# Kernel tuning notes

Measured on AMD Instinct MI355X. Metric: run time of the kernel, lower is better.

The kernel has to match this reference:

```python
import jax, jax.numpy as jnp
import numpy as np

B, N, D = 2, 128, 128          # batch, nodes, dim
DE = 64                        # dim_edge_refinement
H, DH = 8, 32                  # heads, per-head dim
DI = H * DH                    # dim_inner = dim * dim_head = 256
DMI = 2 * DI                   # mlp_expansion_factor * dim_inner = 512
MD = 2                         # max_degree
S = 1 + 2 * MD                 # value/edge channel groups = 5
FFD = 512                      # int(2.0 * dim * 2) for EquivariantFeedForward


def _ln(x, g, eps=1e-5):
    mu = x.mean(-1, keepdims=True)
    var = ((x - mu) ** 2).mean(-1, keepdims=True)
    return (x - mu) / jnp.sqrt(var + eps) * g


def setup_inputs() -> dict:
    key = jax.random.key(0)
    ks = iter(jax.random.split(key, 64))
    def rn(shape, scale=1.0):
        return jax.random.normal(next(ks), shape, dtype=jnp.float32) * scale
    w = 0.05
    return dict(
        h=rn((B, N, D)), x1=rn((B, N, D, 3)), x2=rn((B, N, D, 5)),
        t_ij=rn((B, N, N, D)), r1=rn((B, N, N, 3)), r2=rn((B, N, N, 5)),
        g_i=jnp.ones((D,), jnp.float32), g_j=jnp.ones((D,), jnp.float32),
        Wq=rn((D, DI), w), Wk=rn((D, DI), w),
        Wv1=rn((D, DMI), w), bv1=jnp.zeros((DMI,), jnp.float32),
        Wv2=rn((DMI, S * DI), w), bv2=jnp.zeros((S * DI,), jnp.float32),
        Wp1=rn((D, DMI), w), bp1=jnp.zeros((DMI,), jnp.float32),
        Wp2=rn((DMI, S * DI), w), bp2=jnp.zeros((S * DI,), jnp.float32),
        Wek=rn((D, S * DI), w), Wev=rn((D, S * DI), w),
        Wcomb=rn((DI, D), w),
        Wqh=rn((D, DE), w), Wk1h=rn((D, DE), w), Wk2h=rn((D, DE), w),
        Wep=rn((2 * DE, D), w), Wres=rn((D, D), w),
        P1=rn((D, D), w), P2=rn((D, D), w),
        Wf1a=rn((2 * D, FFD), w), bf1a=jnp.zeros((FFD,), jnp.float32),
        Wf2a=rn((FFD, 2 * D), w), bf2a=jnp.zeros((2 * D,), jnp.float32),
        Wf1b=rn((2 * D, FFD), w), bf1b=jnp.zeros((FFD,), jnp.float32),
        Wf2b=rn((FFD, 2 * D), w), bf2b=jnp.zeros((2 * D,), jnp.float32),
    )


def reference(h, x1, x2, t_ij, r1, r2, g_i, g_j, Wq, Wk, Wv1, bv1, Wv2, bv2,
              Wp1, bp1, Wp2, bp2, Wek, Wev, Wcomb, Wqh, Wk1h, Wk2h, Wep, Wres,
              P1, P2, Wf1a, bf1a, Wf2a, bf2a, Wf1b, bf1b, Wf2b, bf2b):
    # ---- HierarchicalTensorRefinement: per-degree inner products -> edge refresh
    q1 = jnp.einsum('bndm,de->bnem', x1, Wqh)
    q2 = jnp.einsum('bndm,de->bnem', x2, Wqh)
    k1 = jnp.einsum('bndm,de->bnem', x1, Wk1h)
    k2 = jnp.einsum('bndm,de->bnem', x2, Wk2h)
    w_ij = jnp.concatenate([
        jnp.einsum('biem,bjem->bije', q1, k1),
        jnp.einsum('biem,bjem->bije', q2, k2)], axis=-1)       # [b,n,n,2*DE]
    t = w_ij @ Wep + t_ij @ Wres                                # [b,n,n,D]
    # ---- GeometryAwareTensorAttention
    hi = _ln(h, g_i)
    hj = _ln(h, g_j)
    q = (hi @ Wq).reshape(B, N, H, DH).transpose(0, 2, 1, 3)    # bhnd
    k = (hj @ Wk).reshape(B, N, H, DH).transpose(0, 2, 1, 3)
    v = (jax.nn.silu(hj @ Wv1 + bv1) @ Wv2 + bv2).reshape(B, N, S, H, DH).transpose(0, 3, 1, 2, 4)   # bhnsd
    pv = (jax.nn.silu(hj @ Wp1 + bp1) @ Wp2 + bp2).reshape(B, N, S, H, DH).transpose(0, 3, 1, 2, 4)
    ek = jax.nn.silu(t @ Wek).reshape(B, N, N, S, H, DH).transpose(0, 4, 1, 2, 3, 5)                  # bhijsd
    ev = (t @ Wev).reshape(B, N, N, S, H, DH).transpose(0, 4, 1, 2, 3, 5)
    sim_num = jnp.einsum('bhid,bhjd->bhij', q, k)
    sim_den = jnp.einsum('bhid,bhijsd->bhis', q, ek)            # edge-keyed denominator
    attn = sim_num[..., None] / sim_den[:, :, :, None, :]       # bhijs
    sea = attn[..., None] * v[:, :, None] + ev * pv[:, :, None]  # bhijsd
    out = sea.transpose(0, 2, 3, 4, 1, 5).reshape(B, N, N, S, H * DH) @ Wcomb  # [b,i,j,S,D]
    h_sc = out[..., 0, :]              # [b,i,j,D]
    r_sc = out[..., 1:1 + MD, :]       # [b,i,j,MD,D]
    x_sc = out[..., 1 + MD:, :]        # [b,i,j,MD,D]
    h2 = h + h_sc.sum(axis=2)
    x1a = jnp.einsum('bjdm,bijd->bidm', x1, x_sc[..., 0, :]) + jnp.einsum('bijm,bijd->bidm', r1, r_sc[..., 0, :])
    x2a = jnp.einsum('bjdm,bijd->bidm', x2, x_sc[..., 1, :]) + jnp.einsum('bijm,bijd->bidm', r2, r_sc[..., 1, :])
    # ---- EquivariantFeedForward (eq 13)
    def ff_branch(xl, P, W1, b1, W2, b2):
        proj = jnp.einsum('bndm,de->bnem', xl, P)
        inv = jnp.sqrt((proj ** 2).sum(-1) + 1e-12)             # invariant norm over m
        mo = jax.nn.silu(jnp.concatenate([h2, inv], -1) @ W1 + b1) @ W2 + b2
        m1, m2 = jnp.split(mo, 2, axis=-1)
        return m1, proj * m2[..., None]
    m1a, xr1 = ff_branch(x1a, P1, Wf1a, bf1a, Wf2a, bf2a)
    m1b, xr2 = ff_branch(x2a, P2, Wf1b, bf1b, Wf2b, bf2b)
    h3 = h2 + m1a + m1b
    x1f = x1a + xr1
    x2f = x2a + xr2
    # pack outputs: h [b,n,d,1] | x1 [b,n,d,3] | x2 [b,n,d,5] -> [b,n,d,9]
    return jnp.concatenate([h3[..., None], x1f, x2f], axis=-1)
```

## Files before the change

kernel.cpp:

```cpp
#include <hip/hip_runtime.h>
#include <math.h>

#define OFF_Q    0
#define OFF_K    65536
#define OFF_A1V  131072
#define OFF_A1P  262144
#define OFF_V    393216
#define OFF_PV   720896
#define OFF_VW   1048576
#define OFF_QK   2359296
#define OFF_T    2621440
#define OFF_DEN  6815744
#define OFF_ACC  6825984
#define OFF_WEVT 7940096
#define OFF_WCT  8022016
#define OFF_HI   8038400
#define OFF_HJ   8071168

typedef __bf16 bf16x8 __attribute__((ext_vector_type(8)));
typedef float  f32x4  __attribute__((ext_vector_type(4)));

__device__ __forceinline__ float silu_f(float x){
  return x / (1.0f + __expf(-x));
}
__device__ __forceinline__ unsigned short f2bf(float x){
  union{float f; unsigned u;} c; c.f = x;
  unsigned r = c.u + 0x7FFFu + ((c.u >> 16) & 1u);
  return (unsigned short)(r >> 16);
}
__device__ __forceinline__ unsigned packbf(float a, float b){
  return (unsigned)f2bf(a) | ((unsigned)f2bf(b) << 16);
}

__global__ __launch_bounds__(128) void k0a_ln(
    const float* __restrict__ h, const float* __restrict__ g_i, const float* __restrict__ g_j,
    float* __restrict__ ws)
{
  __shared__ float red[2];
  const int r = blockIdx.x, tid = threadIdx.x;
  const int w = tid >> 6, l = tid & 63;
  const float hv = h[r*128 + tid];
  float s = hv;
  #pragma unroll
  for (int o = 1; o < 64; o <<= 1) s += __shfl_xor(s, o);
  if (l == 0) red[w] = s;
  __syncthreads();
  const float mu = (red[0] + red[1]) * (1.f/128.f);
  const float dv = hv - mu;
  float s2 = dv*dv;
  #pragma unroll
  for (int o = 1; o < 64; o <<= 1) s2 += __shfl_xor(s2, o);
  __syncthreads();
  if (l == 0) red[w] = s2;
  __syncthreads();
  const float rstd = 1.0f / sqrtf((red[0] + red[1])*(1.f/128.f) + 1e-5f);
  ws[OFF_HI + r*128 + tid] = dv * rstd * g_i[tid];
  ws[OFF_HJ + r*128 + tid] = dv * rstd * g_j[tid];
  if (tid < 40) ws[OFF_DEN + r*40 + tid] = 0.f;
}

__global__ __launch_bounds__(256) void k0b_qkv(
    const float* __restrict__ Wq, const float* __restrict__ Wk,
    const float* __restrict__ Wv1, const float* __restrict__ bv1,
    const float* __restrict__ Wp1, const float* __restrict__ bp1,
    float* __restrict__ ws)
{
  __shared__ float hrow[128];
  const int bid = blockIdx.x;
  const int row = bid / 6, ch = bid - 6*(bid/6);
  const int tid = threadIdx.x;
  if (tid < 128) hrow[tid] = ws[((ch == 0) ? OFF_HI : OFF_HJ) + row*128 + tid];
  __syncthreads();
  const float* W; int c; float bias = 0.f; bool act = false; float* dst; int wstride;
  switch(ch){
    case 0: W = Wq;  c = tid;      wstride = 256; dst = ws + OFF_Q   + row*256 + c; break;
    case 1: W = Wk;  c = tid;      wstride = 256; dst = ws + OFF_K   + row*256 + c; break;
    case 2: W = Wv1; c = tid;      wstride = 512; bias = bv1[c]; act = true; dst = ws + OFF_A1V + row*512 + c; break;
    case 3: W = Wv1; c = 256+tid;  wstride = 512; bias = bv1[c]; act = true; dst = ws + OFF_A1V + row*512 + c; break;
    case 4: W = Wp1; c = tid;      wstride = 512; bias = bp1[c]; act = true; dst = ws + OFF_A1P + row*512 + c; break;
    default:W = Wp1; c = 256+tid;  wstride = 512; bias = bp1[c]; act = true; dst = ws + OFF_A1P + row*512 + c; break;
  }
  float acc = bias;
  #pragma unroll 8
  for (int d = 0; d < 128; ++d) acc += hrow[d] * W[d*wstride + c];
  *dst = act ? silu_f(acc) : acc;
}

__global__ __launch_bounds__(256) void k0c_qk12(
    const float* __restrict__ x1, const float* __restrict__ x2,
    const float* __restrict__ Wqh, const float* __restrict__ Wk1h, const float* __restrict__ Wk2h,
    float* __restrict__ ws)
{
  __shared__ float x1r[384], x2r[640];
  const int row = blockIdx.x, tid = threadIdx.x;
  for (int idx = tid; idx < 384; idx += 256) x1r[idx] = x1[row*384 + idx];
  for (int idx = tid; idx < 640; idx += 256) x2r[idx] = x2[row*640 + idx];
  __syncthreads();
  for (int idx = tid; idx < 512; idx += 256){
    if (idx < 192){
      const int e = idx/3, m = idx - e*3;
      float qa = 0.f, ka = 0.f;
      #pragma unroll 8
      for (int d = 0; d < 128; ++d){
        const float xv = x1r[d*3 + m];
        qa += xv*Wqh[d*64 + e];
        ka += xv*Wk1h[d*64 + e];
      }
      ws[OFF_QK + row*1024 + idx] = qa;
      ws[OFF_QK + row*1024 + 512 + idx] = ka;
    } else {
      const int i2 = idx - 192;
      const int e = i2/5, m = i2 - e*5;
      float qa = 0.f, ka = 0.f;
      #pragma unroll 8
      for (int d = 0; d < 128; ++d){
        const float xv = x2r[d*5 + m];
        qa += xv*Wqh[d*64 + e];
        ka += xv*Wk2h[d*64 + e];
      }
      ws[OFF_QK + row*1024 + 192 + i2] = qa;
      ws[OFF_QK + row*1024 + 704 + i2] = ka;
    }
  }
}

__global__ __launch_bounds__(256) void k1_vp(
    const float* __restrict__ Wv2, const float* __restrict__ bv2,
    const float* __restrict__ Wp2, const float* __restrict__ bp2,
    float* __restrict__ ws)
{
  __shared__ float A[512][16];
  __shared__ float Bc[64][128];
  const int tid = threadIdx.x;
  const int rt = blockIdx.x & 31;
  const int ct = blockIdx.x >> 5;
  const int r0 = rt*16;
  const bool isP = (r0 >= 256);
  const int rbase = isP ? (r0 - 256) : r0;
  const float* __restrict__ src  = ws + (isP ? OFF_A1P : OFF_A1V);
  const float* __restrict__ W    = isP ? Wp2 : Wv2;
  const float* __restrict__ bias = isP ? bp2 : bv2;
  const int c0 = ct*128;
  for (int idx = tid; idx < 2048; idx += 256){
    const int rl = idx & 15;
    const int c4 = (idx >> 4) * 4;
    const float4 v = *(const float4*)&src[(rbase+rl)*512 + c4];
    A[c4+0][rl] = v.x; A[c4+1][rl] = v.y; A[c4+2][rl] = v.z; A[c4+3][rl] = v.w;
  }
  float acc[4][2] = {{0.f}};
  const int rg = tid & 3;
  const int cg = tid >> 2;
  for (int kc = 0; kc < 8; ++kc){
    __syncthreads();
    for (int idx = tid; idx < 2048; idx += 256){
      const int kl = idx >> 5;
      const int c4 = (idx & 31)*4;
      *(float4*)&Bc[kl][c4] = *(const float4*)&W[(kc*64+kl)*1280 + c0 + c4];
    }
    __syncthreads();
    #pragma unroll 8
    for (int k = 0; k < 64; ++k){
      const float4 a = *(const float4*)&A[kc*64+k][rg*4];
      const float b0 = Bc[k][cg*2], b1 = Bc[k][cg*2+1];
      acc[0][0] += a.x*b0; acc[0][1] += a.x*b1;
      acc[1][0] += a.y*b0; acc[1][1] += a.y*b1;
      acc[2][0] += a.z*b0; acc[2][1] += a.z*b1;
      acc[3][0] += a.w*b0; acc[3][1] += a.w*b1;
    }
  }
  float* __restrict__ dst = ws + (isP ? OFF_PV : OFF_V);
  for (int rr = 0; rr < 4; ++rr)
    for (int cc = 0; cc < 2; ++cc){
      const int c = c0 + cg*2 + cc;
      dst[(rbase + rg*4 + rr)*1280 + c] = acc[rr][cc] + bias[c];
    }
}

__global__ __launch_bounds__(256) void k2_vw(const float* __restrict__ Wcomb, float* __restrict__ ws)
{
  __shared__ float vr[1280];
  const int j = blockIdx.x, tid = threadIdx.x;
  for (int idx = tid; idx < 320; idx += 256)
    *(float4*)&vr[idx*4] = *(const float4*)&ws[OFF_V + j*1280 + idx*4];
  __syncthreads();
  const int d = tid & 127;
  for (int sh = tid >> 7; sh < 40; sh += 2){
    const int s = sh >> 3, hh = sh & 7;
    float a = 0.f;
    #pragma unroll 8
    for (int dh = 0; dh < 32; ++dh)
      a += vr[s*256 + hh*32 + dh] * Wcomb[(hh*32+dh)*128 + d];
    ws[OFF_VW + j*5120 + sh*128 + d] = a;
  }
}

__global__ __launch_bounds__(256) void k_cvt(
    const float* __restrict__ Wev, const float* __restrict__ Wcomb, float* __restrict__ ws)
{
  __shared__ float ld[16][256];
  const int tid = threadIdx.x;
  if (blockIdx.x < 80){
    const int c0 = blockIdx.x*16;
    for (int p = 0; p < 8; ++p){
      const int idx = tid + p*256;
      const int k = idx >> 4, cl = idx & 15;
      ld[cl][k] = Wev[k*1280 + c0 + cl];
    }
    __syncthreads();
    const int cl = tid >> 4, k8 = tid & 15;
    uint4 u;
    u.x = packbf(ld[cl][k8*8+0], ld[cl][k8*8+1]);
    u.y = packbf(ld[cl][k8*8+2], ld[cl][k8*8+3]);
    u.z = packbf(ld[cl][k8*8+4], ld[cl][k8*8+5]);
    u.w = packbf(ld[cl][k8*8+6], ld[cl][k8*8+7]);
    ((uint4*)(ws + OFF_WEVT))[(c0+cl)*16 + k8] = u;
  } else {
    const int c0 = (blockIdx.x - 80)*16;
    for (int p = 0; p < 16; ++p){
      const int idx = tid + p*256;
      const int k = idx >> 4, cl = idx & 15;
      ld[cl][k] = Wcomb[k*128 + c0 + cl];
    }
    __syncthreads();
    const int cl = tid >> 4, k8i = tid & 15;
    for (int pass = 0; pass < 2; ++pass){
      const int k8 = k8i + pass*16;
      uint4 u;
      u.x = packbf(ld[cl][k8*8+0], ld[cl][k8*8+1]);
      u.y = packbf(ld[cl][k8*8+2], ld[cl][k8*8+3]);
      u.z = packbf(ld[cl][k8*8+4], ld[cl][k8*8+5]);
      u.w = packbf(ld[cl][k8*8+6], ld[cl][k8*8+7]);
      ((uint4*)(ws + OFF_WCT))[(c0+cl)*32 + k8] = u;
    }
  }
}

__global__ __launch_bounds__(512) void k3_t(
    const float* __restrict__ t_ij, const float* __restrict__ Wep, const float* __restrict__ Wres,
    float* __restrict__ ws)
{
  __shared__ float A[256][64];
  __shared__ float bufB[8192];
  __shared__ float qrow[512];
  const int tid = threadIdx.x;
  const int bi = blockIdx.x >> 1;
  const int jt = blockIdx.x & 1;
  const int j0 = jt*64;
  const int b  = bi >> 7;
  if (tid < 128) *(float4*)&qrow[tid*4] = *(const float4*)&ws[OFF_QK + bi*1024 + tid*4];
  for (int idx = tid; idx < 2048; idx += 512){
    const int jl = idx >> 5;
    const int d4 = (idx & 31)*4;
    const float4 v = *(const float4*)&t_ij[(bi*128 + j0 + jl)*128 + d4];
    A[128+d4+0][jl] = v.x; A[128+d4+1][jl] = v.y; A[128+d4+2][jl] = v.z; A[128+d4+3][jl] = v.w;
  }
  float* kst = bufB;
  for (int jq = 0; jq < 4; ++jq){
    __syncthreads();
    for (int idx = tid; idx < 2048; idx += 512){
      const int jl = idx & 15;
      const int c4 = (idx >> 4)*4;
      const float4 v = *(const float4*)&ws[OFF_QK + (b*128 + j0 + jq*16 + jl)*1024 + 512 + c4];
      kst[(c4+0)*16 + jl] = v.x; kst[(c4+1)*16 + jl] = v.y;
      kst[(c4+2)*16 + jl] = v.z; kst[(c4+3)*16 + jl] = v.w;
    }
    __syncthreads();
    for (int idx = tid; idx < 2048; idx += 512){
      const int jl = idx & 15;
      const int e  = idx >> 4;
      float acc = 0.f;
      if (e < 64){
        #pragma unroll
        for (int m = 0; m < 3; ++m) acc += qrow[e*3+m] * kst[(e*3+m)*16 + jl];
      } else {
        const int e2 = e - 64;
        #pragma unroll
        for (int m = 0; m < 5; ++m) acc += qrow[192 + e2*5+m] * kst[(192 + e2*5+m)*16 + jl];
      }
      A[e][jq*16 + jl] = acc;
    }
  }
  float acc[4][4] = {{0.f}};
  const int jg = tid & 15;
  const int cg = tid >> 4;
  float* Bc = bufB;
  for (int kc = 0; kc < 4; ++kc){
    __syncthreads();
    for (int idx = tid; idx < 2048; idx += 512){
      const int kl = idx >> 5;
      const int c4 = (idx & 31)*4;
      const int k = kc*64 + kl;
      const float* srcw = (k < 128) ? &Wep[k*128 + c4] : &Wres[(k-128)*128 + c4];
      *(float4*)&Bc[kl*128 + c4] = *(const float4*)srcw;
    }
    __syncthreads();
    #pragma unroll 2
    for (int kl = 0; kl < 64; ++kl){
      const float4 a = *(const float4*)&A[kc*64+kl][jg*4];
      const float2 bA = *(const float2*)&Bc[kl*128 + cg*2];
      const float2 bB = *(const float2*)&Bc[kl*128 + 64 + cg*2];
      const float av[4] = {a.x,a.y,a.z,a.w};
      #pragma unroll
      for (int r = 0; r < 4; ++r){
        acc[r][0] += av[r]*bA.x; acc[r][1] += av[r]*bA.y;
        acc[r][2] += av[r]*bB.x; acc[r][3] += av[r]*bB.y;
      }
    }
  }
  __syncthreads();
  for (int jj = 0; jj < 4; ++jj){
    bufB[(jg*4+jj)*128 + cg*2+0]    = acc[jj][0];
    bufB[(jg*4+jj)*128 + cg*2+1]    = acc[jj][1];
    bufB[(jg*4+jj)*128 + 64+cg*2+0] = acc[jj][2];
    bufB[(jg*4+jj)*128 + 64+cg*2+1] = acc[jj][3];
  }
  __syncthreads();
  for (int idx = tid; idx < 2048; idx += 512){
    const int jl = idx >> 5;
    const int c4 = (idx & 31)*4;
    *(float4*)&ws[OFF_T + (bi*128 + j0 + jl)*128 + c4] = *(const float4*)&bufB[jl*128 + c4];
  }
}

__global__ __launch_bounds__(256) void k4_den(
    const float* __restrict__ Wek, float* __restrict__ ws)
{
  __shared__ float tl[128][64];
  __shared__ float wl[128][64];
  __shared__ float den[40];
  __shared__ float ql[256];
  const int tid = threadIdx.x;
  const int bi = blockIdx.x >> 1;
  const int jh = blockIdx.x & 1;
  const int j0 = jh*64;
  for (int idx = tid; idx < 2048; idx += 256){
    const int jl = idx >> 5;
    const int c4 = (idx & 31)*4;
    const float4 v = *(const float4*)&ws[OFF_T + (bi*128 + j0 + jl)*128 + c4];
    tl[c4+0][jl] = v.x; tl[c4+1][jl] = v.y; tl[c4+2][jl] = v.z; tl[c4+3][jl] = v.w;
  }
  if (tid < 40) den[tid] = 0.f;
  ql[tid] = ws[OFF_Q + bi*256 + tid];
  const int jg = tid & 15;
  const int cg = tid >> 4;
  for (int ch = 0; ch < 20; ++ch){
    __syncthreads();
    for (int idx = tid; idx < 2048; idx += 256){
      const int kl = idx >> 4;
      const int c4 = (idx & 15)*4;
      *(float4*)&wl[kl][c4] = *(const float4*)&Wek[kl*1280 + ch*64 + c4];
    }
    __syncthreads();
    float acc[4][4] = {{0.f}};
    #pragma unroll 2
    for (int k = 0; k < 128; ++k){
      const float4 a = *(const float4*)&tl[k][jg*4];
      const float4 w = *(const float4*)&wl[k][cg*4];
      const float av[4] = {a.x,a.y,a.z,a.w};
      #pragma unroll
      for (int r = 0; r < 4; ++r){
        acc[r][0] += av[r]*w.x; acc[r][1] += av[r]*w.y;
        acc[r][2] += av[r]*w.z; acc[r][3] += av[r]*w.w;
      }
    }
    #pragma unroll
    for (int cc = 0; cc < 4; ++cc){
      const int col = ch*64 + cg*4 + cc;
      float cs = silu_f(acc[0][cc]) + silu_f(acc[1][cc]) + silu_f(acc[2][cc]) + silu_f(acc[3][cc]);
      cs += __shfl_xor(cs, 1, 16);
      cs += __shfl_xor(cs, 2, 16);
      cs += __shfl_xor(cs, 4, 16);
      cs += __shfl_xor(cs, 8, 16);
      if (jg == 0){
        const int s  = col >> 8;
        const int hd = col & 255;
        atomicAdd(&den[(hd>>5)*5 + s], ql[hd]*cs);
      }
    }
  }
  __syncthreads();
  if (tid < 40) atomicAdd(&ws[OFF_DEN + bi*40 + tid], den[tid]);
}

__global__ __launch_bounds__(512, 4) void k5_pass2(
    const float* __restrict__ x1, const float* __restrict__ x2,
    const float* __restrict__ r1, const float* __restrict__ r2,
    float* __restrict__ ws)
{
  __shared__ unsigned short tA[8192];
  __shared__ unsigned short wevB[8192];
  __shared__ unsigned short wcombB[8192];
  __shared__ unsigned short epB[4096];
  __shared__ float num[8][64];
  __shared__ float acc17[17*128];
  __shared__ float ql[256];
  __shared__ float rdenl[40];

  const int tid  = threadIdx.x;
  const int lane = tid & 63;
  const int w    = tid >> 6;
  const int wm   = w & 3;
  const int wn   = w >> 2;
  const int l15  = lane & 15;
  const int kq   = lane >> 4;

  const int bi = blockIdx.x >> 1;
  const int jh = blockIdx.x & 1;
  const int j0 = jh*64;
  const int b  = bi >> 7;

  #pragma unroll
  for (int p = 0; p < 4; ++p){
    const int idx = tid + p*512;
    const int j = idx >> 5;
    const int d4 = (idx & 31)*4;
    const float4 v = *(const float4*)&ws[OFF_T + (bi*128 + j0 + j)*128 + d4];
    uint2 u;
    u.x = packbf(v.x, v.y);
    u.y = packbf(v.z, v.w);
    *(uint2*)((char*)tA + j*256 + ((d4*2) ^ ((j&7)<<4))) = u;
  }
  if (tid < 64) *(float4*)&ql[tid*4] = *(const float4*)&ws[OFF_Q + bi*256 + tid*4];
  if (tid < 40) rdenl[tid] = 1.0f / ws[OFF_DEN + bi*40 + tid];
  for (int idx = tid; idx < 17*128; idx += 512) acc17[idx] = 0.f;
  __syncthreads();

  {
    const int hh = tid >> 6, jl = tid & 63;
    const float* krow = &ws[OFF_K + (b*128 + j0 + jl)*256 + hh*32];
    float a = 0.f;
    #pragma unroll
    for (int dh = 0; dh < 32; ++dh) a += ql[hh*32+dh]*krow[dh];
    num[hh][jl] = a;
  }

  const int jA = wm*16 + l15;
  bf16x8 af[4];
  #pragma unroll
  for (int ks = 0; ks < 4; ++ks)
    af[ks] = *(const bf16x8*)((const char*)tA + jA*256 + ((ks*64 + kq*16) ^ ((jA&7)<<4)));

  const uint4* wevt = (const uint4*)(ws + OFF_WEVT);
  const uint4* wct  = (const uint4*)(ws + OFF_WCT);

  for (int s = 0; s < 5; ++s){
    f32x4 o0 = {0,0,0,0}, o1 = {0,0,0,0}, o2 = {0,0,0,0}, o3 = {0,0,0,0};
    for (int ch4 = 0; ch4 < 4; ++ch4){
      __syncthreads();
      #pragma unroll
      for (int p = 0; p < 2; ++p){
        const int idx = tid + p*512;
        const int cl = idx & 63, kg = idx >> 6;
        const uint4 v = wevt[(s*256 + ch4*64 + cl)*16 + kg];
        *(uint4*)((char*)wevB + cl*256 + ((kg*16) ^ ((cl&7)<<4))) = v;
      }
      #pragma unroll
      for (int p = 0; p < 2; ++p){
        const int idx = tid + p*512;
        const int hg = idx & 7, d = idx >> 3;
        const uint4 v = wct[d*32 + ch4*8 + hg];
        *(uint4*)((char*)wcombB + d*128 + ((hg*16) ^ ((d&7)<<4))) = v;
      }
      __syncthreads();
      f32x4 ev0 = {0,0,0,0}, ev1 = {0,0,0,0};
      {
        const int c0l = wn*32 + l15;
        const int c1l = c0l + 16;
        #pragma unroll
        for (int ks = 0; ks < 4; ++ks){
          const bf16x8 b0 = *(const bf16x8*)((const char*)wevB + c0l*256 + ((ks*64 + kq*16) ^ ((c0l&7)<<4)));
          const bf16x8 b1 = *(const bf16x8*)((const char*)wevB + c1l*256 + ((ks*64 + kq*16) ^ ((c1l&7)<<4)));
          ev0 = __builtin_amdgcn_mfma_f32_16x16x32_bf16(af[ks], b0, ev0, 0, 0, 0);
          ev1 = __builtin_amdgcn_mfma_f32_16x16x32_bf16(af[ks], b1, ev1, 0, 0, 0);
        }
      }
      #pragma unroll
      for (int nt = 0; nt < 2; ++nt){
        const int cl = wn*32 + nt*16 + l15;
        const int cglob = s*256 + ch4*64 + cl;
        #pragma unroll
        for (int r = 0; r < 4; ++r){
          const int jl = wm*16 + kq*4 + r;
          const float pvv = ws[OFF_PV + (b*128 + j0 + jl)*1280 + cglob];
          const float evv = (nt == 0) ? ev0[r] : ev1[r];
          *(unsigned short*)((char*)epB + jl*128 + ((cl*2) ^ ((jl&7)<<4))) = f2bf(evv * pvv);
        }
      }
      __syncthreads();
      #pragma unroll
      for (int ks = 0; ks < 2; ++ks){
        const bf16x8 a = *(const bf16x8*)((const char*)epB + jA*128 + ((ks*64 + kq*16) ^ ((jA&7)<<4)));
        #pragma unroll
        for (int nt = 0; nt < 4; ++nt){
          const int dl = wn*64 + nt*16 + l15;
          const bf16x8 bb = *(const bf16x8*)((const char*)wcombB + dl*128 + ((ks*64 + kq*16) ^ ((dl&7)<<4)));
          if      (nt == 0) o0 = __builtin_amdgcn_mfma_f32_16x16x32_bf16(a, bb, o0, 0, 0, 0);
          else if (nt == 1) o1 = __builtin_amdgcn_mfma_f32_16x16x32_bf16(a, bb, o1, 0, 0, 0);
          else if (nt == 2) o2 = __builtin_amdgcn_mfma_f32_16x16x32_bf16(a, bb, o2, 0, 0, 0);
          else              o3 = __builtin_amdgcn_mfma_f32_16x16x32_bf16(a, bb, o3, 0, 0, 0);
        }
      }
    }
    #pragma unroll
    for (int r = 0; r < 4; ++r){
      const int jl = wm*16 + kq*4 + r;
      const float* vwbase = ws + OFF_VW + (b*128 + j0 + jl)*5120 + s*1024 + wn*64 + l15;
      #pragma unroll
      for (int hh = 0; hh < 8; ++hh){
        const float at = num[hh][jl] * rdenl[hh*5 + s];
        const float* vp = vwbase + hh*128;
        o0[r] += at * vp[0];
        o1[r] += at * vp[16];
        o2[r] += at * vp[32];
        o3[r] += at * vp[48];
      }
    }
    if (s == 0){
      #pragma unroll
      for (int nt = 0; nt < 4; ++nt){
        const f32x4 oo = (nt==0)?o0:(nt==1)?o1:(nt==2)?o2:o3;
        float p = oo[0] + oo[1] + oo[2] + oo[3];
        p += __shfl_xor(p, 16);
        p += __shfl_xor(p, 32);
        if (lane < 16) atomicAdd(&acc17[wn*64 + nt*16 + lane], p);
      }
    } else if (s <= 2){
      const int M = (s == 1) ? 3 : 5;
      const int slot0 = (s == 1) ? 1 : 4;
      const float* rw = (s == 1) ? r1 : r2;
      for (int m = 0; m < M; ++m){
        float wj[4];
        #pragma unroll
        for (int r = 0; r < 4; ++r)
          wj[r] = rw[(bi*128 + j0 + wm*16 + kq*4 + r)*M + m];
        #pragma unroll
        for (int nt = 0; nt < 4; ++nt){
          const f32x4 oo = (nt==0)?o0:(nt==1)?o1:(nt==2)?o2:o3;
          float p = wj[0]*oo[0] + wj[1]*oo[1] + wj[2]*oo[2] + wj[3]*oo[3];
          p += __shfl_xor(p, 16);
          p += __shfl_xor(p, 32);
          if (lane < 16) atomicAdd(&acc17[(slot0+m)*128 + wn*64 + nt*16 + lane], p);
        }
      }
    } else {
      const int M = (s == 3) ? 3 : 5;
      const int slot0 = (s == 3) ? 9 : 12;
      const float* xw = (s == 3) ? x1 : x2;
      for (int m = 0; m < M; ++m){
        #pragma unroll
        for (int nt = 0; nt < 4; ++nt){
          const int d = wn*64 + nt*16 + l15;
          const f32x4 oo = (nt==0)?o0:(nt==1)?o1:(nt==2)?o2:o3;
          float p = 0.f;
          #pragma unroll
          for (int r = 0; r < 4; ++r)
            p += xw[((b*128 + j0 + wm*16 + kq*4 + r)*128 + d)*M + m] * oo[r];
          p += __shfl_xor(p, 16);
          p += __shfl_xor(p, 32);
          if (lane < 16) atomicAdd(&acc17[(slot0+m)*128 + d], p);
        }
      }
    }
  }
  __syncthreads();
  for (int idx = tid; idx < 2176; idx += 512)
    ws[OFF_ACC + (bi*2 + jh)*2176 + idx] = acc17[idx];
}

__global__ __launch_bounds__(256) void k6_tail(
    const float* __restrict__ h,
    const float* __restrict__ P1, const float* __restrict__ P2,
    const float* __restrict__ Wf1a, const float* __restrict__ bf1a,
    const float* __restrict__ Wf2a, const float* __restrict__ bf2a,
    const float* __restrict__ Wf1b, const float* __restrict__ bf1b,
    const float* __restrict__ Wf2b, const float* __restrict__ bf2b,
    const float* __restrict__ ws, float* __restrict__ out)
{
  __shared__ float a17[2176];
  __shared__ float h2s[128];
  __shared__ float x1a[384], x2a[640];
  __shared__ float pj1[384], pj2[640];
  __shared__ float inv1[128], inv2[128];
  __shared__ float za[512], zb[512];
  __shared__ float m1a[128], m2a[128], m1b[128], m2b[128];
  const int tid = threadIdx.x;
  const int row = blockIdx.x;
  for (int idx = tid; idx < 2176; idx += 256)
    a17[idx] = ws[OFF_ACC + (row*2)*2176 + idx] + ws[OFF_ACC + (row*2+1)*2176 + idx];
  __syncthreads();
  if (tid < 128) h2s[tid] = h[row*128 + tid] + a17[tid];
  for (int idx = tid; idx < 384; idx += 256){
    const int d = idx/3, m = idx - d*3;
    x1a[idx] = a17[(1+m)*128 + d] + a17[(9+m)*128 + d];
  }
  for (int idx = tid; idx < 640; idx += 256){
    const int d = idx/5, m = idx - d*5;
    x2a[idx] = a17[(4+m)*128 + d] + a17[(12+m)*128 + d];
  }
  __syncthreads();
  if (tid < 128){
    const int e = tid;
    float pa[3] = {0.f,0.f,0.f};
    for (int d = 0; d < 128; ++d){
      const float p = P1[d*128 + e];
      pa[0] += x1a[d*3+0]*p;
      pa[1] += x1a[d*3+1]*p;
      pa[2] += x1a[d*3+2]*p;
    }
    pj1[e*3+0] = pa[0]; pj1[e*3+1] = pa[1]; pj1[e*3+2] = pa[2];
    inv1[e] = sqrtf(pa[0]*pa[0] + pa[1]*pa[1] + pa[2]*pa[2] + 1e-12f);
  } else {
    const int e = tid - 128;
    float pa[5] = {0.f,0.f,0.f,0.f,0.f};
    for (int d = 0; d < 128; ++d){
      const float p = P2[d*128 + e];
      pa[0] += x2a[d*5+0]*p;
      pa[1] += x2a[d*5+1]*p;
      pa[2] += x2a[d*5+2]*p;
      pa[3] += x2a[d*5+3]*p;
      pa[4] += x2a[d*5+4]*p;
    }
    #pragma unroll
    for (int m = 0; m < 5; ++m) pj2[e*5+m] = pa[m];
    inv2[e] = sqrtf(pa[0]*pa[0]+pa[1]*pa[1]+pa[2]*pa[2]+pa[3]*pa[3]+pa[4]*pa[4] + 1e-12f);
  }
  __syncthreads();
  for (int it = 0; it < 2; ++it){
    const int f = tid + it*256;
    float av = bf1a[f], bv_ = bf1b[f];
    #pragma unroll 4
    for (int k = 0; k < 128; ++k){
      av  += h2s[k]*Wf1a[k*512 + f];
      bv_ += h2s[k]*Wf1b[k*512 + f];
    }
    #pragma unroll 4
    for (int k = 0; k < 128; ++k){
      av  += inv1[k]*Wf1a[(128+k)*512 + f];
      bv_ += inv2[k]*Wf1b[(128+k)*512 + f];
    }
    za[f] = silu_f(av); zb[f] = silu_f(bv_);
  }
  __syncthreads();
  {
    const int g = tid;
    float am = bf2a[g], bm = bf2b[g];
    #pragma unroll 4
    for (int f = 0; f < 512; ++f){
      am += za[f]*Wf2a[f*256 + g];
      bm += zb[f]*Wf2b[f*256 + g];
    }
    if (g < 128){ m1a[g] = am; m1b[g] = bm; }
    else        { m2a[g-128] = am; m2b[g-128] = bm; }
  }
  __syncthreads();
  if (tid < 128){
    const int d = tid;
    const int ob = (row*128 + d)*9;
    out[ob+0] = h2s[d] + m1a[d] + m1b[d];
    #pragma unroll
    for (int m = 0; m < 3; ++m)
      out[ob+1+m] = x1a[d*3+m] + pj1[d*3+m]*m2a[d];
    #pragma unroll
    for (int m = 0; m < 5; ++m)
      out[ob+4+m] = x2a[d*5+m] + pj2[d*5+m]*m2b[d];
  }
}

extern "C" void kernel_launch(void* const* d_in, const int* in_sizes, int n_in,
                              void* d_out, int out_size, void* d_ws, size_t ws_size,
                              hipStream_t stream)
{
  (void)in_sizes; (void)n_in; (void)out_size; (void)ws_size;
  const float* h    = (const float*)d_in[0];
  const float* x1   = (const float*)d_in[1];
  const float* x2   = (const float*)d_in[2];
  const float* t_ij = (const float*)d_in[3];
  const float* r1   = (const float*)d_in[4];
  const float* r2   = (const float*)d_in[5];
  const float* g_i  = (const float*)d_in[6];
  const float* g_j  = (const float*)d_in[7];
  const float* Wq   = (const float*)d_in[8];
  const float* Wk   = (const float*)d_in[9];
  const float* Wv1  = (const float*)d_in[10];
  const float* bv1  = (const float*)d_in[11];
  const float* Wv2  = (const float*)d_in[12];
  const float* bv2  = (const float*)d_in[13];
  const float* Wp1  = (const float*)d_in[14];
  const float* bp1  = (const float*)d_in[15];
  const float* Wp2  = (const float*)d_in[16];
  const float* bp2  = (const float*)d_in[17];
  const float* Wek  = (const float*)d_in[18];
  const float* Wev  = (const float*)d_in[19];
  const float* Wcomb= (const float*)d_in[20];
  const float* Wqh  = (const float*)d_in[21];
  const float* Wk1h = (const float*)d_in[22];
  const float* Wk2h = (const float*)d_in[23];
  const float* Wep  = (const float*)d_in[24];
  const float* Wres = (const float*)d_in[25];
  const float* P1   = (const float*)d_in[26];
  const float* P2   = (const float*)d_in[27];
  const float* Wf1a = (const float*)d_in[28];
  const float* bf1a = (const float*)d_in[29];
  const float* Wf2a = (const float*)d_in[30];
  const float* bf2a = (const float*)d_in[31];
  const float* Wf1b = (const float*)d_in[32];
  const float* bf1b = (const float*)d_in[33];
  const float* Wf2b = (const float*)d_in[34];
  const float* bf2b = (const float*)d_in[35];
  float* ws  = (float*)d_ws;
  float* out = (float*)d_out;

  k0a_ln <<<dim3(256),  dim3(128), 0, stream>>>(h, g_i, g_j, ws);
  k0b_qkv<<<dim3(1536), dim3(256), 0, stream>>>(Wq, Wk, Wv1, bv1, Wp1, bp1, ws);
  k0c_qk12<<<dim3(256), dim3(256), 0, stream>>>(x1, x2, Wqh, Wk1h, Wk2h, ws);
  k1_vp  <<<dim3(320),  dim3(256), 0, stream>>>(Wv2, bv2, Wp2, bp2, ws);
  k2_vw  <<<dim3(256),  dim3(256), 0, stream>>>(Wcomb, ws);
  k_cvt  <<<dim3(88),   dim3(256), 0, stream>>>(Wev, Wcomb, ws);
  k3_t   <<<dim3(512),  dim3(512), 0, stream>>>(t_ij, Wep, Wres, ws);
  k4_den <<<dim3(512),  dim3(256), 0, stream>>>(Wek, ws);
  k5_pass2<<<dim3(512), dim3(512), 0, stream>>>(x1, x2, r1, r2, ws);
  k6_tail<<<dim3(256),  dim3(256), 0, stream>>>(h, P1, P2, Wf1a, bf1a, Wf2a, bf2a, Wf1b, bf1b, Wf2b, bf2b, ws, out);
}
```

Before: 746.9 us.

## Restructure edge GEMMs with swizzled LDS and register-streamed weights, split den over columns

k3_t and k4_den now keep only the activation tile in shared memory, using an XOR-swizzled layout to avoid bank conflicts. Weights are read straight from global memory with one-step register prefetch instead of being staged through LDS. k4_den is split across five 256-column groups, giving a 2560-block grid with 64 accumulators per thread, and the per-head reductions are done in shared memory before the global atomics. The aim is to cut LDS traffic and barriers and raise parallelism, at the cost of more register pressure and repeated global weight reads per block.

```diff
diff --git a/kernel.cpp b/kernel.cpp
--- a/kernel.cpp
+++ b/kernel.cpp
@@ -30,6 +30,12 @@
 }
 __device__ __forceinline__ unsigned packbf(float a, float b){
   return (unsigned)f2bf(a) | ((unsigned)f2bf(b) << 16);
+}
+__device__ __forceinline__ void swz_store(float* Abase, int k, int j, float v){
+  *(float*)((char*)Abase + k*256 + ((((j>>2) ^ ((k>>2)&15))) << 4) + ((j&3)<<2)) = v;
+}
+__device__ __forceinline__ f32x4 swz_load4(const float* Abase, int k, int chunk){
+  return *(const f32x4*)((const char*)Abase + k*256 + ((chunk ^ ((k>>2)&15)) << 4));
 }
 
 __global__ __launch_bounds__(128) void k0a_ln(
@@ -235,26 +241,19 @@
   }
 }
 
-__global__ __launch_bounds__(512) void k3_t(
+__global__ __launch_bounds__(512, 2) void k3_t(
     const float* __restrict__ t_ij, const float* __restrict__ Wep, const float* __restrict__ Wres,
     float* __restrict__ ws)
 {
-  __shared__ float A[256][64];
-  __shared__ float bufB[8192];
+  __shared__ float A[16384];
   __shared__ float qrow[512];
+  float* kst = A + 8192;
   const int tid = threadIdx.x;
   const int bi = blockIdx.x >> 1;
   const int jt = blockIdx.x & 1;
   const int j0 = jt*64;
   const int b  = bi >> 7;
   if (tid < 128) *(float4*)&qrow[tid*4] = *(const float4*)&ws[OFF_QK + bi*1024 + tid*4];
-  for (int idx = tid; idx < 2048; idx += 512){
-    const int jl = idx >> 5;
-    const int d4 = (idx & 31)*4;
-    const float4 v = *(const float4*)&t_ij[(bi*128 + j0 + jl)*128 + d4];
-    A[128+d4+0][jl] = v.x; A[128+d4+1][jl] = v.y; A[128+d4+2][jl] = v.z; A[128+d4+3][jl] = v.w;
-  }
-  float* kst = bufB;
   for (int jq = 0; jq < 4; ++jq){
     __syncthreads();
     for (int idx = tid; idx < 2048; idx += 512){
@@ -277,109 +276,115 @@
         #pragma unroll
         for (int m = 0; m < 5; ++m) acc += qrow[192 + e2*5+m] * kst[(192 + e2*5+m)*16 + jl];
       }
-      A[e][jq*16 + jl] = acc;
-    }
-  }
-  float acc[4][4] = {{0.f}};
-  const int jg = tid & 15;
-  const int cg = tid >> 4;
-  float* Bc = bufB;
-  for (int kc = 0; kc < 4; ++kc){
-    __syncthreads();
-    for (int idx = tid; idx < 2048; idx += 512){
-      const int kl = idx >> 5;
-      const int c4 = (idx & 31)*4;
-      const int k = kc*64 + kl;
-      const float* srcw = (k < 128) ? &Wep[k*128 + c4] : &Wres[(k-128)*128 + c4];
-      *(float4*)&Bc[kl*128 + c4] = *(const float4*)srcw;
-    }
-    __syncthreads();
-    #pragma unroll 2
-    for (int kl = 0; kl < 64; ++kl){
-      const float4 a = *(const float4*)&A[kc*64+kl][jg*4];
-      const float2 bA = *(const float2*)&Bc[kl*128 + cg*2];
-      const float2 bB = *(const float2*)&Bc[kl*128 + 64 + cg*2];
-      const float av[4] = {a.x,a.y,a.z,a.w};
-      #pragma unroll
-      for (int r = 0; r < 4; ++r){
-        acc[r][0] += av[r]*bA.x; acc[r][1] += av[r]*bA.y;
-        acc[r][2] += av[r]*bB.x; acc[r][3] += av[r]*bB.y;
-      }
-    }
-  }
-  __syncthreads();
-  for (int jj = 0; jj < 4; ++jj){
-    bufB[(jg*4+jj)*128 + cg*2+0]    = acc[jj][0];
-    bufB[(jg*4+jj)*128 + cg*2+1]    = acc[jj][1];
-    bufB[(jg*4+jj)*128 + 64+cg*2+0] = acc[jj][2];
-    bufB[(jg*4+jj)*128 + 64+cg*2+1] = acc[jj][3];
+      swz_store(A, e, jq*16 + jl, acc);
+    }
   }
   __syncthreads();
   for (int idx = tid; idx < 2048; idx += 512){
     const int jl = idx >> 5;
-    const int c4 = (idx & 31)*4;
-    *(float4*)&ws[OFF_T + (bi*128 + j0 + jl)*128 + c4] = *(const float4*)&bufB[jl*128 + c4];
-  }
-}
-
-__global__ __launch_bounds__(256) void k4_den(
+    const int d4 = (idx & 31)*4;
+    const float4 v = *(const float4*)&t_ij[(bi*128 + j0 + jl)*128 + d4];
+    swz_store(A, 128+d4+0, jl, v.x);
+    swz_store(A, 128+d4+1, jl, v.y);
+    swz_store(A, 128+d4+2, jl, v.z);
+    swz_store(A, 128+d4+3, jl, v.w);
+  }
+  __syncthreads();
+  const int jg = tid >> 5;
+  const int cg = tid & 31;
+  f32x4 acc[4] = {{0,0,0,0},{0,0,0,0},{0,0,0,0},{0,0,0,0}};
+  {
+    const float* Wp = Wep + cg*4;
+    f32x4 wv = *(const f32x4*)Wp;
+    for (int k = 0; k < 127; ++k){
+      const f32x4 wn = *(const f32x4*)(Wp + (k+1)*128);
+      const f32x4 av = swz_load4(A, k, jg);
+      acc[0] += wv*av[0]; acc[1] += wv*av[1]; acc[2] += wv*av[2]; acc[3] += wv*av[3];
+      wv = wn;
+    }
+    const f32x4 av = swz_load4(A, 127, jg);
+    acc[0] += wv*av[0]; acc[1] += wv*av[1]; acc[2] += wv*av[2]; acc[3] += wv*av[3];
+  }
+  {
+    const float* Wp = Wres + cg*4;
+    f32x4 wv = *(const f32x4*)Wp;
+    for (int k = 0; k < 127; ++k){
+      const f32x4 wn = *(const f32x4*)(Wp + (k+1)*128);
+      const f32x4 av = swz_load4(A, 128+k, jg);
+      acc[0] += wv*av[0]; acc[1] += wv*av[1]; acc[2] += wv*av[2]; acc[3] += wv*av[3];
+      wv = wn;
+    }
+    const f32x4 av = swz_load4(A, 255, jg);
+    acc[0] += wv*av[0]; acc[1] += wv*av[1]; acc[2] += wv*av[2]; acc[3] += wv*av[3];
+  }
+  #pragma unroll
+  for (int jj = 0; jj < 4; ++jj)
+    *(f32x4*)&ws[OFF_T + (bi*128 + j0 + jg*4 + jj)*128 + cg*4] = acc[jj];
+}
+
+__global__ __launch_bounds__(256, 4) void k4_den(
     const float* __restrict__ Wek, float* __restrict__ ws)
 {
-  __shared__ float tl[128][64];
-  __shared__ float wl[128][64];
-  __shared__ float den[40];
-  __shared__ float ql[256];
+  __shared__ float tl[8192];
+  __shared__ float colsum[4][256];
+  __shared__ float den40[40];
   const int tid = threadIdx.x;
-  const int bi = blockIdx.x >> 1;
-  const int jh = blockIdx.x & 1;
+  const int bid = blockIdx.x;
+  const int bi = bid / 10;
+  const int rem = bid - bi*10;
+  const int jh = rem & 1;
+  const int cq = rem >> 1;
   const int j0 = jh*64;
   for (int idx = tid; idx < 2048; idx += 256){
-    const int jl = idx >> 5;
-    const int c4 = (idx & 31)*4;
-    const float4 v = *(const float4*)&ws[OFF_T + (bi*128 + j0 + jl)*128 + c4];
-    tl[c4+0][jl] = v.x; tl[c4+1][jl] = v.y; tl[c4+2][jl] = v.z; tl[c4+3][jl] = v.w;
-  }
-  if (tid < 40) den[tid] = 0.f;
-  ql[tid] = ws[OFF_Q + bi*256 + tid];
-  const int jg = tid & 15;
-  const int cg = tid >> 4;
-  for (int ch = 0; ch < 20; ++ch){
-    __syncthreads();
-    for (int idx = tid; idx < 2048; idx += 256){
-      const int kl = idx >> 4;
-      const int c4 = (idx & 15)*4;
-      *(float4*)&wl[kl][c4] = *(const float4*)&Wek[kl*1280 + ch*64 + c4];
-    }
-    __syncthreads();
-    float acc[4][4] = {{0.f}};
-    #pragma unroll 2
-    for (int k = 0; k < 128; ++k){
-      const float4 a = *(const float4*)&tl[k][jg*4];
-      const float4 w = *(const float4*)&wl[k][cg*4];
-      const float av[4] = {a.x,a.y,a.z,a.w};
-      #pragma unroll
-      for (int r = 0; r < 4; ++r){
-        acc[r][0] += av[r]*w.x; acc[r][1] += av[r]*w.y;
-        acc[r][2] += av[r]*w.z; acc[r][3] += av[r]*w.w;
-      }
-    }
+    const int j = idx >> 5;
+    const int d4 = (idx & 31)*4;
+    const float4 v = *(const float4*)&ws[OFF_T + (bi*128 + j0 + j)*128 + d4];
+    swz_store(tl, d4+0, j, v.x);
+    swz_store(tl, d4+1, j, v.y);
+    swz_store(tl, d4+2, j, v.z);
+    swz_store(tl, d4+3, j, v.w);
+  }
+  if (tid < 40) den40[tid] = 0.f;
+  __syncthreads();
+  const int w = tid >> 6;
+  const int lane = tid & 63;
+  const float* wekp = Wek + cq*256 + lane*4;
+  f32x4 acc[16];
+  #pragma unroll
+  for (int i = 0; i < 16; ++i) acc[i] = (f32x4){0,0,0,0};
+  f32x4 wv = *(const f32x4*)wekp;
+  for (int k = 0; k < 127; ++k){
+    const f32x4 wn = *(const f32x4*)(wekp + (k+1)*1280);
     #pragma unroll
-    for (int cc = 0; cc < 4; ++cc){
-      const int col = ch*64 + cg*4 + cc;
-      float cs = silu_f(acc[0][cc]) + silu_f(acc[1][cc]) + silu_f(acc[2][cc]) + silu_f(acc[3][cc]);
-      cs += __shfl_xor(cs, 1, 16);
-      cs += __shfl_xor(cs, 2, 16);
-      cs += __shfl_xor(cs, 4, 16);
-      cs += __shfl_xor(cs, 8, 16);
-      if (jg == 0){
-        const int s  = col >> 8;
-        const int hd = col & 255;
-        atomicAdd(&den[(hd>>5)*5 + s], ql[hd]*cs);
-      }
-    }
-  }
-  __syncthreads();
-  if (tid < 40) atomicAdd(&ws[OFF_DEN + bi*40 + tid], den[tid]);
+    for (int q = 0; q < 4; ++q){
+      const f32x4 tv = swz_load4(tl, k, w*4 + q);
+      acc[q*4+0] += wv*tv[0]; acc[q*4+1] += wv*tv[1];
+      acc[q*4+2] += wv*tv[2]; acc[q*4+3] += wv*tv[3];
+    }
+    wv = wn;
+  }
+  #pragma unroll
+  for (int q = 0; q < 4; ++q){
+    const f32x4 tv = swz_load4(tl, 127, w*4 + q);
+    acc[q*4+0] += wv*tv[0]; acc[q*4+1] += wv*tv[1];
+    acc[q*4+2] += wv*tv[2]; acc[q*4+3] += wv*tv[3];
+  }
+  f32x4 cs = {0,0,0,0};
+  #pragma unroll
+  for (int i = 0; i < 16; ++i){
+    #pragma unroll
+    for (int cc = 0; cc < 4; ++cc) cs[cc] += silu_f(acc[i][cc]);
+  }
+  *(f32x4*)&colsum[w][lane*4] = cs;
+  __syncthreads();
+  {
+    const int c = tid;
+    const float v = (colsum[0][c] + colsum[1][c] + colsum[2][c] + colsum[3][c])
+                    * ws[OFF_Q + bi*256 + c];
+    atomicAdd(&den40[(c>>5)*5 + cq], v);
+  }
+  __syncthreads();
+  if (tid < 8) atomicAdd(&ws[OFF_DEN + bi*40 + tid*5 + cq], den40[tid*5 + cq]);
 }
 
 __global__ __launch_bounds__(512, 4) void k5_pass2(
@@ -717,7 +722,7 @@
   k2_vw  <<<dim3(256),  dim3(256), 0, stream>>>(Wcomb, ws);
   k_cvt  <<<dim3(88),   dim3(256), 0, stream>>>(Wev, Wcomb, ws);
   k3_t   <<<dim3(512),  dim3(512), 0, stream>>>(t_ij, Wep, Wres, ws);
-  k4_den <<<dim3(512),  dim3(256), 0, stream>>>(Wek, ws);
+  k4_den <<<dim3(2560), dim3(256), 0, stream>>>(Wek, ws);
   k5_pass2<<<dim3(512), dim3(512), 0, stream>>>(x1, x2, r1, r2, ws);
   k6_tail<<<dim3(256),  dim3(256), 0, stream>>>(h, P1, P2, Wf1a, bf1a, Wf2a, bf2a, Wf1b, bf1b, Wf2b, bf2b, ws, out);
 }
```

New measurement: 1.754 ms. 2.35x slower.
